# Performance work log

Hardware: AMD Instinct MI355X
Metric: run time of the kernel (lower is better)

## Reference

```python
import jax, jax.numpy as jnp
import numpy as np

B, T, V, E, H, C = 128, 512, 100000, 100, 128, 3


def _lstm_dir(xs, w_ih, w_hh, b, reverse=False):
    # xs: [T,B,D]; w_ih: [4H,D]; w_hh: [4H,H]; b: [4H] (b_ih+b_hh combined)
    Tn, Bn, _ = xs.shape
    Hn = w_hh.shape[1]
    if reverse:
        xs = xs[::-1]
    gx = jnp.einsum('tbd,gd->tbg', xs, w_ih) + b  # [T,B,4H] input projections

    def step(carry, g_in):
        h, c = carry
        gates = g_in + h @ w_hh.T
        i, f, g, o = jnp.split(gates, 4, axis=-1)  # torch gate order i,f,g,o
        i = jax.nn.sigmoid(i)
        f = jax.nn.sigmoid(f)
        g = jnp.tanh(g)
        o = jax.nn.sigmoid(o)
        c = f * c + i * g
        h = o * jnp.tanh(c)
        return (h, c), h

    init = (jnp.zeros((Bn, Hn), xs.dtype), jnp.zeros((Bn, Hn), xs.dtype))
    (h_last, _), hs = jax.lax.scan(step, init, gx)
    if reverse:
        hs = hs[::-1]
    return hs, h_last


def setup_inputs() -> dict:
    key = jax.random.key(0)
    ks = jax.random.split(key, 24)
    s_e = 1.0 / np.sqrt(H)

    def u(k, shape):
        return jax.random.uniform(k, shape, jnp.float32, -s_e, s_e)

    x = jax.random.randint(ks[0], (B, T), 0, V, dtype=jnp.int32)
    emb = jax.random.normal(ks[1], (V, E), jnp.float32)
    emb = emb.at[0].set(0.0)  # padding_idx=0
    inp = {'x': x, 'emb': emb}
    names = []
    idx = 2
    for layer, din in ((0, E), (1, 2 * H)):
        for suf in ('', 'r'):
            inp[f'w_ih_l{layer}{suf}'] = u(ks[idx], (4 * H, din)); idx += 1
            inp[f'w_hh_l{layer}{suf}'] = u(ks[idx], (4 * H, H)); idx += 1
            inp[f'b_ih_l{layer}{suf}'] = u(ks[idx], (4 * H,)); idx += 1
            inp[f'b_hh_l{layer}{suf}'] = u(ks[idx], (4 * H,)); idx += 1
    s_f = 1.0 / np.sqrt(2 * H)
    inp['fc_w'] = jax.random.uniform(ks[22], (C, 2 * H), jnp.float32, -s_f, s_f)
    inp['fc_b'] = jax.random.uniform(ks[23], (C,), jnp.float32, -s_f, s_f)
    return inp


def reference(x, emb, w_ih_l0, w_hh_l0, b_ih_l0, b_hh_l0,
              w_ih_l0r, w_hh_l0r, b_ih_l0r, b_hh_l0r,
              w_ih_l1, w_hh_l1, b_ih_l1, b_hh_l1,
              w_ih_l1r, w_hh_l1r, b_ih_l1r, b_hh_l1r,
              fc_w, fc_b):
    # dropout is identity in eval mode
    xe = emb[x]                      # [B,T,E]
    xs = jnp.transpose(xe, (1, 0, 2))  # [T,B,E]
    # layer 0 bidirectional
    hf0, _ = _lstm_dir(xs, w_ih_l0, w_hh_l0, b_ih_l0 + b_hh_l0, reverse=False)
    hb0, _ = _lstm_dir(xs, w_ih_l0r, w_hh_l0r, b_ih_l0r + b_hh_l0r, reverse=True)
    x1 = jnp.concatenate([hf0, hb0], axis=-1)  # [T,B,2H]
    # layer 1 bidirectional; only final hidden states needed
    _, hF = _lstm_dir(x1, w_ih_l1, w_hh_l1, b_ih_l1 + b_hh_l1, reverse=False)
    _, hB = _lstm_dir(x1, w_ih_l1r, w_hh_l1r, b_ih_l1r + b_hh_l1r, reverse=True)
    out = jnp.concatenate([hF, hB], axis=1)  # [B,2H] == cat(hidden[-2], hidden[-1])
    return out @ fc_w.T + fc_b  # [B,C]
```

## Files before the change

kernel.cpp:

```cpp
#include <hip/hip_runtime.h>
#include <hip/hip_bf16.h>
#include <math.h>

#define TT 512
#define BB 128
#define EE 100
#define HH 128
#define G4 512
#define K1 256

typedef __attribute__((ext_vector_type(8))) short bf16x8;
typedef __attribute__((ext_vector_type(4))) float f32x4;

__device__ inline unsigned short bf16_rne(float v) {
    __hip_bfloat16 h = __float2bfloat16(v);
    return *reinterpret_cast<unsigned short*>(&h);
}

template<int CTRL>
__device__ inline float dppf(float x) {
    int r = __builtin_amdgcn_update_dpp(0, __float_as_int(x), CTRL, 0xF, 0xF, true);
    return __int_as_float(r);
}

__device__ inline float sig_fast(float z) {
    return __builtin_amdgcn_rcpf(1.f + __expf(-z));
}

__global__ void embed_cvt(const int* __restrict__ x, const float* __restrict__ emb,
                          unsigned short* __restrict__ xs2) {
    int row = blockIdx.x;
    int k = threadIdx.x;
    int b = row & 127, t = row >> 7;
    int tok = x[b * TT + t];
    float v = (k < EE) ? emb[(size_t)tok * EE + k] : 0.f;
    xs2[(size_t)row * 128 + k] = bf16_rne(v);
}

__global__ void wcvt2(const float* __restrict__ srcf, const float* __restrict__ srcr,
                      int Kin, int Kp,
                      unsigned short* __restrict__ dstf, unsigned short* __restrict__ dstr) {
    const float* src = blockIdx.y ? srcr : srcf;
    unsigned short* dst = blockIdx.y ? dstr : dstf;
    int n = blockIdx.x;
    int k = threadIdx.x;
    int j = n & 3;
    int gate = ((j & 1) << 1) | (j >> 1);
    int r = gate * 128 + (n >> 2);
    float v = (k < Kin) ? src[(size_t)r * Kin + k] : 0.f;
    dst[(size_t)n * Kp + k] = bf16_rne(v);
}

__global__ void bias2(const float* __restrict__ bihf0, const float* __restrict__ bhhf0,
                      const float* __restrict__ bihr0, const float* __restrict__ bhhr0,
                      const float* __restrict__ bihf1, const float* __restrict__ bhhf1,
                      const float* __restrict__ bihr1, const float* __restrict__ bhhr1,
                      float* __restrict__ dst) {
    int n = blockIdx.x * 256 + threadIdx.x;
    int layer = n >> 10;
    int d = (n >> 9) & 1, m = n & 511;
    int j = m & 3;
    int gate = ((j & 1) << 1) | (j >> 1);
    int src = gate * 128 + (m >> 2);
    const float* a = layer ? (d ? bihr1 : bihf1) : (d ? bihr0 : bihf0);
    const float* c = layer ? (d ? bhhr1 : bhhf1) : (d ? bhhr0 : bhhf0);
    dst[n] = a[src] + c[src];
}

__global__ void whh_pack4(const float* __restrict__ w0f, const float* __restrict__ w0r,
                          const float* __restrict__ w1f, const float* __restrict__ w1r,
                          float* __restrict__ dstbase) {
    int which = blockIdx.y;
    const float* src = which == 0 ? w0f : which == 1 ? w0r : which == 2 ? w1f : w1r;
    float* dst = dstbase + (size_t)which * 128 * 128 * 4;
    int u = blockIdx.x;
    int k = threadIdx.x;
    float4 v;
    v.x = src[((size_t)(0 * 128 + u)) * 128 + k];
    v.y = src[((size_t)(1 * 128 + u)) * 128 + k];
    v.z = src[((size_t)(2 * 128 + u)) * 128 + k];
    v.w = src[((size_t)(3 * 128 + u)) * 128 + k];
    reinterpret_cast<float4*>(dst)[(size_t)u * 128 + k] = v;
}

template<int K2>
__global__ __launch_bounds__(512, 1) void lstm_fused(
    const unsigned short* __restrict__ A2,
    const unsigned short* __restrict__ W2,
    const float* __restrict__ biascat,
    const float* __restrict__ wpkf,
    const float* __restrict__ wpkr,
    unsigned short* __restrict__ out_x1,
    float* __restrict__ hlast)
{
    constexpr int S = 64;
    constexpr int NCH = TT / S;
    constexpr int NKT = K2 / 32;

    __shared__ float gxl[512 * 65];
    __shared__ float hb[2][160];

    int blk = blockIdx.x;
    int dir = blk >> 7;
    int b   = blk & 127;
    const float* wpk = dir ? wpkr : wpkf;
    int tid = threadIdx.x;
    int u = tid >> 2, q = tid & 3;
    int lane = tid & 63, w = tid >> 6;
    int l15 = lane & 15, g = lane >> 4;

    const f32x4* wp4 = reinterpret_cast<const f32x4*>(wpk) + ((size_t)u * 128 + q * 32);
#define LW(i) const f32x4 w##i = wp4[i];
    LW(0)  LW(1)  LW(2)  LW(3)  LW(4)  LW(5)  LW(6)  LW(7)
    LW(8)  LW(9)  LW(10) LW(11) LW(12) LW(13) LW(14) LW(15)
    LW(16) LW(17) LW(18) LW(19) LW(20) LW(21) LW(22) LW(23)
    LW(24) LW(25) LW(26) LW(27) LW(28) LW(29) LW(30) LW(31)
#undef LW

    const unsigned short* wbase[4];
    float biasr[4];
    #pragma unroll
    for (int k = 0; k < 4; ++k) {
        int n = (4 * w + k) * 16 + l15;
        wbase[k] = W2 + (size_t)(dir * 512 + n) * K2 + g * 8;
        biasr[k] = biascat[dir * 512 + n];
    }

    int hslot = (u >> 5) * 40 + (u & 31);
    float h = 0.f, c = 0.f;
    if (q == 0) hb[0][hslot] = 0.f;

    bool odd2 = (q & 2) != 0;
    bool oddq = (q & 1) != 0;
    float fq = (q == 1) ? 2.f : 1.f;
    float bq = (q == 1) ? -1.f : 0.f;
    float* gxrow = &gxl[tid * 65];

    for (int ch = 0; ch < NCH; ++ch) {
        __syncthreads();
        const unsigned short* abase[4];
        #pragma unroll
        for (int m = 0; m < 4; ++m) {
            int sg = ch * S + m * 16 + l15;
            int t = dir ? (TT - 1 - sg) : sg;
            abase[m] = A2 + ((size_t)t * BB + b) * K2 + g * 8;
        }
        #pragma unroll
        for (int p = 0; p < 2; ++p) {
            f32x4 acc[4][2];
            const f32x4 z = {0.f, 0.f, 0.f, 0.f};
            #pragma unroll
            for (int m = 0; m < 4; ++m) {
                acc[m][0] = z; acc[m][1] = z;
            }
            #pragma unroll
            for (int kt = 0; kt < NKT; ++kt) {
                bf16x8 af[4], bfr[2];
                #pragma unroll
                for (int m = 0; m < 4; ++m)
                    af[m] = *reinterpret_cast<const bf16x8*>(abase[m] + kt * 32);
                #pragma unroll
                for (int jj = 0; jj < 2; ++jj)
                    bfr[jj] = *reinterpret_cast<const bf16x8*>(wbase[2 * p + jj] + kt * 32);
                #pragma unroll
                for (int m = 0; m < 4; ++m)
                    #pragma unroll
                    for (int jj = 0; jj < 2; ++jj)
                        acc[m][jj] = __builtin_amdgcn_mfma_f32_16x16x32_bf16(
                            af[m], bfr[jj], acc[m][jj], 0, 0, 0);
            }
            #pragma unroll
            for (int m = 0; m < 4; ++m)
                #pragma unroll
                for (int jj = 0; jj < 2; ++jj) {
                    int col = (4 * w + 2 * p + jj) * 16 + l15;
                    int s0 = m * 16 + g * 4;
                    float bv = biasr[2 * p + jj];
                    #pragma unroll
                    for (int r = 0; r < 4; ++r)
                        gxl[col * 65 + s0 + r] = acc[m][jj][r] + bv;
                }
        }
        __syncthreads();
        for (int sl = 0; sl < S; ++sl) {
            int p2 = sl & 1;
            float gin = gxrow[sl];

            const float4* hb4 = reinterpret_cast<const float4*>(&hb[p2][40 * q]);
            float4 hv0 = hb4[0], hv1 = hb4[1], hv2 = hb4[2], hv3 = hb4[3];
            float4 hv4 = hb4[4], hv5 = hb4[5], hv6 = hb4[6], hv7 = hb4[7];

            f32x4 a0 = {0.f,0.f,0.f,0.f}, a1 = {0.f,0.f,0.f,0.f};
            f32x4 a2 = {0.f,0.f,0.f,0.f}, a3 = {0.f,0.f,0.f,0.f};
#define FM(i0,i1,i2,i3,HV) { \
            f32x4 hh; \
            hh = f32x4{HV.x,HV.x,HV.x,HV.x}; a0 = __builtin_elementwise_fma(w##i0, hh, a0); \
            hh = f32x4{HV.y,HV.y,HV.y,HV.y}; a1 = __builtin_elementwise_fma(w##i1, hh, a1); \
            hh = f32x4{HV.z,HV.z,HV.z,HV.z}; a2 = __builtin_elementwise_fma(w##i2, hh, a2); \
            hh = f32x4{HV.w,HV.w,HV.w,HV.w}; a3 = __builtin_elementwise_fma(w##i3, hh, a3); }
            FM(0,1,2,3,hv0)     FM(4,5,6,7,hv1)     FM(8,9,10,11,hv2)   FM(12,13,14,15,hv3)
            FM(16,17,18,19,hv4) FM(20,21,22,23,hv5) FM(24,25,26,27,hv6) FM(28,29,30,31,hv7)
#undef FM
            f32x4 acc = (a0 + a1) + (a2 + a3);

            float xs = acc.x + dppf<0xB1>(acc.x);
            float ys = acc.y + dppf<0xB1>(acc.y);
            float zs = acc.z + dppf<0xB1>(acc.z);
            float ws = acc.w + dppf<0xB1>(acc.w);
            float sa = oddq ? zs : xs;
            float sb = oddq ? ws : ys;
            float sa2 = sa + dppf<0x4E>(sa);
            float sb2 = sb + dppf<0x4E>(sb);
            float pre_dot = odd2 ? sb2 : sa2;

            float pre = pre_dot + gin;
            float act = __builtin_fmaf(sig_fast(pre * fq), fq, bq);

            float ig = dppf<0x00>(act);
            float gg = dppf<0x55>(act);
            float fg = dppf<0xAA>(act);
            float og = dppf<0xFF>(act);

            c = fg * c + ig * gg;
            float th = __builtin_fmaf(2.f, sig_fast(2.f * c), -1.f);
            h = og * th;

            if (q == 0) {
                hb[p2 ^ 1][hslot] = h;
                if (out_x1) {
                    int tg = dir ? (TT - 1 - (ch * S + sl)) : (ch * S + sl);
                    out_x1[((size_t)tg * BB + b) * 256 + dir * HH + u] = bf16_rne(h);
                }
            }
            asm volatile("s_waitcnt lgkmcnt(0)" ::: "memory");
            __builtin_amdgcn_s_barrier();
            asm volatile("" ::: "memory");
        }
    }
    if (hlast && q == 0)
        hlast[(dir * BB + b) * HH + u] = h;
}

__global__ void fc_kernel(const float* __restrict__ h_state,
                          const float* __restrict__ fc_w,
                          const float* __restrict__ fc_b,
                          float* __restrict__ out) {
    int tid = blockIdx.x * blockDim.x + threadIdx.x;
    if (tid >= BB * 3) return;
    int b = tid / 3;
    int c = tid % 3;
    float acc = 0.f;
    for (int j = 0; j < 256; ++j) {
        float v = (j < HH) ? h_state[((size_t)0 * BB + b) * HH + j]
                           : h_state[((size_t)1 * BB + b) * HH + (j - HH)];
        acc += v * fc_w[c * 256 + j];
    }
    out[b * 3 + c] = acc + fc_b[c];
}

extern "C" void kernel_launch(void* const* d_in, const int* in_sizes, int n_in,
                              void* d_out, int out_size, void* d_ws, size_t ws_size,
                              hipStream_t stream) {
    const int*   x        = (const int*)  d_in[0];
    const float* emb      = (const float*)d_in[1];
    const float* w_ih_l0  = (const float*)d_in[2];
    const float* w_hh_l0  = (const float*)d_in[3];
    const float* b_ih_l0  = (const float*)d_in[4];
    const float* b_hh_l0  = (const float*)d_in[5];
    const float* w_ih_l0r = (const float*)d_in[6];
    const float* w_hh_l0r = (const float*)d_in[7];
    const float* b_ih_l0r = (const float*)d_in[8];
    const float* b_hh_l0r = (const float*)d_in[9];
    const float* w_ih_l1  = (const float*)d_in[10];
    const float* w_hh_l1  = (const float*)d_in[11];
    const float* b_ih_l1  = (const float*)d_in[12];
    const float* b_hh_l1  = (const float*)d_in[13];
    const float* w_ih_l1r = (const float*)d_in[14];
    const float* w_hh_l1r = (const float*)d_in[15];
    const float* b_ih_l1r = (const float*)d_in[16];
    const float* b_hh_l1r = (const float*)d_in[17];
    const float* fc_w     = (const float*)d_in[18];
    const float* fc_b     = (const float*)d_in[19];
    float* out = (float*)d_out;
    (void)in_sizes; (void)n_in; (void)out_size; (void)ws_size;

    size_t xs2_b   = (size_t)TT * BB * 128 * 2;
    size_t x1_b    = (size_t)TT * BB * 256 * 2;
    size_t w2l0_b  = (size_t)512 * 128 * 2;
    size_t w2l1_b  = (size_t)512 * 256 * 2;
    size_t bias_b  = (size_t)1024 * 4;
    size_t wpk_b   = (size_t)128 * 128 * 4 * 4;
    size_t state_b = (size_t)2 * BB * HH * 4;
    char* ws = (char*)d_ws;
    size_t off = 0;
    unsigned short* xs2   = (unsigned short*)(ws + off); off += xs2_b;
    unsigned short* x1_2  = (unsigned short*)(ws + off); off += x1_b;
    unsigned short* w2l0f = (unsigned short*)(ws + off); off += w2l0_b;
    unsigned short* w2l0r = (unsigned short*)(ws + off); off += w2l0_b;
    unsigned short* w2l1f = (unsigned short*)(ws + off); off += w2l1_b;
    unsigned short* w2l1r = (unsigned short*)(ws + off); off += w2l1_b;
    float* biasl0  = (float*)(ws + off); off += bias_b;
    float* biasl1  = (float*)(ws + off); off += bias_b;
    float* wpk0f   = (float*)(ws + off); off += wpk_b;
    float* wpk0r   = (float*)(ws + off); off += wpk_b;
    float* wpk1f   = (float*)(ws + off); off += wpk_b;
    float* wpk1r   = (float*)(ws + off); off += wpk_b;
    float* h_state = (float*)(ws + off); off += state_b;

    embed_cvt<<<TT * BB, 128, 0, stream>>>(x, emb, xs2);
    wcvt2<<<dim3(512, 2), 128, 0, stream>>>(w_ih_l0, w_ih_l0r, EE, 128, w2l0f, w2l0r);
    wcvt2<<<dim3(512, 2), 256, 0, stream>>>(w_ih_l1, w_ih_l1r, K1, 256, w2l1f, w2l1r);
    bias2<<<8, 256, 0, stream>>>(b_ih_l0, b_hh_l0, b_ih_l0r, b_hh_l0r,
                                 b_ih_l1, b_hh_l1, b_ih_l1r, b_hh_l1r, biasl0);
    whh_pack4<<<dim3(128, 4), 128, 0, stream>>>(w_hh_l0, w_hh_l0r, w_hh_l1, w_hh_l1r, wpk0f);

    lstm_fused<128><<<256, 512, 0, stream>>>(xs2, w2l0f, biasl0, wpk0f, wpk0r,
                                             x1_2, nullptr);
    lstm_fused<256><<<256, 512, 0, stream>>>(x1_2, w2l1f, biasl1, wpk1f, wpk1r,
                                             nullptr, h_state);
    fc_kernel<<<2, 192, 0, stream>>>(h_state, fc_w, fc_b, out);
}
```

Before: 870.5 us.

## Stage input chunk in swizzled LDS via global_load_lds and single-pass MFMA

The per-chunk input projection now loads each chunk of the A activations into LDS once with direct global-to-LDS loads and an XOR swizzle. Before, every wave re-read the same A rows from global memory in two passes. The four gate column groups are now computed in one pass with more accumulators. Layer 1 uses a smaller chunk of 32 timesteps so the staged tile fits in the fixed 1024-entry LDS buffer. This cuts redundant global traffic but adds an extra barrier per chunk and more accumulator registers.

```diff
diff --git a/kernel.cpp b/kernel.cpp
--- a/kernel.cpp
+++ b/kernel.cpp
@@ -15,6 +15,12 @@
 __device__ inline unsigned short bf16_rne(float v) {
     __hip_bfloat16 h = __float2bfloat16(v);
     return *reinterpret_cast<unsigned short*>(&h);
+}
+
+__device__ inline void gload16(const void* g, void* l) {
+    __builtin_amdgcn_global_load_lds(
+        (const __attribute__((address_space(1))) void*)g,
+        (__attribute__((address_space(3))) void*)l, 16, 0, 0);
 }
 
 template<int CTRL>
@@ -83,7 +89,7 @@
     reinterpret_cast<float4*>(dst)[(size_t)u * 128 + k] = v;
 }
 
-template<int K2>
+template<int K2, int S, int STRIDE>
 __global__ __launch_bounds__(512, 1) void lstm_fused(
     const unsigned short* __restrict__ A2,
     const unsigned short* __restrict__ W2,
@@ -93,11 +99,13 @@
     unsigned short* __restrict__ out_x1,
     float* __restrict__ hlast)
 {
-    constexpr int S = 64;
     constexpr int NCH = TT / S;
     constexpr int NKT = K2 / 32;
-
-    __shared__ float gxl[512 * 65];
+    constexpr int CPR = K2 / 8;
+    constexpr int M   = S / 16;
+
+    __shared__ float gxl[512 * STRIDE];
+    __shared__ bf16x8 Asl[1024];
     __shared__ float hb[2][160];
 
     int blk = blockIdx.x;
@@ -134,51 +142,57 @@
     bool oddq = (q & 1) != 0;
     float fq = (q == 1) ? 2.f : 1.f;
     float bq = (q == 1) ? -1.f : 0.f;
-    float* gxrow = &gxl[tid * 65];
+    float* gxrow = &gxl[tid * STRIDE];
 
     for (int ch = 0; ch < NCH; ++ch) {
         __syncthreads();
-        const unsigned short* abase[4];
         #pragma unroll
-        for (int m = 0; m < 4; ++m) {
-            int sg = ch * S + m * 16 + l15;
+        for (int j = 0; j < 2; ++j) {
+            int slot = tid + j * 512;
+            int row = slot / CPR;
+            int cl = slot % CPR;
+            int cs = cl ^ (row & 7);
+            int sg = ch * S + row;
             int t = dir ? (TT - 1 - sg) : sg;
-            abase[m] = A2 + ((size_t)t * BB + b) * K2 + g * 8;
+            gload16(A2 + ((size_t)t * BB + b) * K2 + cs * 8, &Asl[slot]);
         }
-        #pragma unroll
-        for (int p = 0; p < 2; ++p) {
-            f32x4 acc[4][2];
+        __syncthreads();
+        {
+            f32x4 acc[M][4];
             const f32x4 z = {0.f, 0.f, 0.f, 0.f};
             #pragma unroll
-            for (int m = 0; m < 4; ++m) {
-                acc[m][0] = z; acc[m][1] = z;
+            for (int m = 0; m < M; ++m)
+                #pragma unroll
+                for (int cg = 0; cg < 4; ++cg) acc[m][cg] = z;
+            #pragma unroll
+            for (int kt = 0; kt < NKT; ++kt) {
+                bf16x8 bfr[4], af[M];
+                #pragma unroll
+                for (int cg = 0; cg < 4; ++cg)
+                    bfr[cg] = *reinterpret_cast<const bf16x8*>(wbase[cg] + kt * 32);
+                #pragma unroll
+                for (int m = 0; m < M; ++m) {
+                    int row = m * 16 + l15;
+                    int cc = (kt * 4 + g) ^ (row & 7);
+                    af[m] = Asl[row * CPR + cc];
+                }
+                #pragma unroll
+                for (int m = 0; m < M; ++m)
+                    #pragma unroll
+                    for (int cg = 0; cg < 4; ++cg)
+                        acc[m][cg] = __builtin_amdgcn_mfma_f32_16x16x32_bf16(
+                            af[m], bfr[cg], acc[m][cg], 0, 0, 0);
             }
             #pragma unroll
-            for (int kt = 0; kt < NKT; ++kt) {
-                bf16x8 af[4], bfr[2];
-                #pragma unroll
-                for (int m = 0; m < 4; ++m)
-                    af[m] = *reinterpret_cast<const bf16x8*>(abase[m] + kt * 32);
-                #pragma unroll
-                for (int jj = 0; jj < 2; ++jj)
-                    bfr[jj] = *reinterpret_cast<const bf16x8*>(wbase[2 * p + jj] + kt * 32);
-                #pragma unroll
-                for (int m = 0; m < 4; ++m)
-                    #pragma unroll
-                    for (int jj = 0; jj < 2; ++jj)
-                        acc[m][jj] = __builtin_amdgcn_mfma_f32_16x16x32_bf16(
-                            af[m], bfr[jj], acc[m][jj], 0, 0, 0);
-            }
-            #pragma unroll
-            for (int m = 0; m < 4; ++m)
-                #pragma unroll
-                for (int jj = 0; jj < 2; ++jj) {
-                    int col = (4 * w + 2 * p + jj) * 16 + l15;
+            for (int m = 0; m < M; ++m)
+                #pragma unroll
+                for (int cg = 0; cg < 4; ++cg) {
+                    int col = (4 * w + cg) * 16 + l15;
                     int s0 = m * 16 + g * 4;
-                    float bv = biasr[2 * p + jj];
+                    float bv = biasr[cg];
                     #pragma unroll
                     for (int r = 0; r < 4; ++r)
-                        gxl[col * 65 + s0 + r] = acc[m][jj][r] + bv;
+                        gxl[col * STRIDE + s0 + r] = acc[m][cg][r] + bv;
                 }
         }
         __syncthreads();
@@ -314,9 +328,9 @@
                                  b_ih_l1, b_hh_l1, b_ih_l1r, b_hh_l1r, biasl0);
     whh_pack4<<<dim3(128, 4), 128, 0, stream>>>(w_hh_l0, w_hh_l0r, w_hh_l1, w_hh_l1r, wpk0f);
 
-    lstm_fused<128><<<256, 512, 0, stream>>>(xs2, w2l0f, biasl0, wpk0f, wpk0r,
-                                             x1_2, nullptr);
-    lstm_fused<256><<<256, 512, 0, stream>>>(x1_2, w2l1f, biasl1, wpk1f, wpk1r,
-                                             nullptr, h_state);
+    lstm_fused<128, 64, 65><<<256, 512, 0, stream>>>(xs2, w2l0f, biasl0, wpk0f, wpk0r,
+                                                     x1_2, nullptr);
+    lstm_fused<256, 32, 33><<<256, 512, 0, stream>>>(x1_2, w2l1f, biasl1, wpk1f, wpk1r,
+                                                     nullptr, h_state);
     fc_kernel<<<2, 192, 0, stream>>>(h_state, fc_w, fc_b, out);
 }
```

Result: faster. 789.0 us (-9.4%).
